# Kernel tuning notes

Hardware: AMD Instinct MI355X
Metric: run time of the kernel (lower is better)

## Reference

```python
import jax, jax.numpy as jnp
import numpy as np
from jax import lax

HEAD_DIM = 8          # attention_head_dim
EPS_ATTN = 1e-15
EPS_RMS = 1e-5
KPAD = 2              # kernel_size 5 -> padding 2


def setup_inputs() -> dict:
    key = jax.random.key(0)
    ks = jax.random.split(key, 9)
    B, C, H, W = 2, 1152, 64, 64
    inner = 1152                     # num_heads(144) * head_dim(8)
    ch3 = 3 * inner                  # 3456
    s = 0.02
    return {
        "hidden_states": jax.random.normal(ks[0], (B, C, H, W), jnp.float32),
        "Wq": jax.random.normal(ks[1], (inner, C), jnp.float32) * s,
        "Wk": jax.random.normal(ks[2], (inner, C), jnp.float32) * s,
        "Wv": jax.random.normal(ks[3], (inner, C), jnp.float32) * s,
        "proj_in_w": jax.random.normal(ks[4], (ch3, 1, 5, 5), jnp.float32) * s,   # depthwise 5x5
        "proj_out_w": jax.random.normal(ks[5], (ch3, HEAD_DIM, 1, 1), jnp.float32) * s,  # grouped 1x1, groups=3*heads
        "Wout": jax.random.normal(ks[6], (C, 2 * inner), jnp.float32) * s,
        "rms_w": jnp.ones((C,), jnp.float32),
        "rms_b": jnp.zeros((C,), jnp.float32),
    }


def reference(hidden_states, Wq, Wk, Wv, proj_in_w, proj_out_w, Wout, rms_w, rms_b):
    x = hidden_states
    B, C, H, W = x.shape
    xh = jnp.transpose(x, (0, 2, 3, 1))                      # BHWC
    q = xh @ Wq.T
    k = xh @ Wk.T
    v = xh @ Wv.T
    qkv = jnp.transpose(jnp.concatenate([q, k, v], axis=-1), (0, 3, 1, 2))  # B,3*inner,H,W
    ch = qkv.shape[1]
    # multiscale branch: depthwise 5x5 then grouped 1x1 (groups = 3*num_heads)
    ms = lax.conv_general_dilated(qkv, proj_in_w, (1, 1), [(KPAD, KPAD), (KPAD, KPAD)],
                                  dimension_numbers=("NCHW", "OIHW", "NCHW"),
                                  feature_group_count=ch)
    ms = lax.conv_general_dilated(ms, proj_out_w, (1, 1), [(0, 0), (0, 0)],
                                  dimension_numbers=("NCHW", "OIHW", "NCHW"),
                                  feature_group_count=ch // HEAD_DIM)
    hs = jnp.concatenate([qkv, ms], axis=1).astype(jnp.float32)   # B, 2*3*inner, H, W
    hs = hs.reshape(B, -1, 3 * HEAD_DIM, H * W)                   # B, G, 3d, N
    q2, k2, v2 = jnp.split(hs, 3, axis=2)                         # each B,G,d,N
    q2 = jax.nn.relu(q2)
    k2 = jax.nn.relu(k2)
    # linear attention: pad value with a ones row (for the normalizer)
    v_pad = jnp.concatenate([v2, jnp.ones_like(v2[:, :, :1])], axis=2)  # B,G,d+1,N
    scores = jnp.einsum("bgdn,bgen->bgde", v_pad, k2)             # B,G,d+1,d (tiny)
    out = jnp.einsum("bgde,bgen->bgdn", scores, q2)               # B,G,d+1,N
    out = out[:, :, :-1] / (out[:, :, -1:] + EPS_ATTN)            # normalize by last row
    out = out.reshape(B, -1, H, W)                                # B, 2*inner, H, W
    out = jnp.transpose(out, (0, 2, 3, 1)) @ Wout.T               # BHW,C_out
    # RMSNorm over channel (last) dim, with affine weight + bias
    ms2 = jnp.mean(out * out, axis=-1, keepdims=True)
    out = out * lax.rsqrt(ms2 + EPS_RMS) * rms_w + rms_b
    return jnp.transpose(out, (0, 3, 1, 2))
```

## Files before the change

### kernel.cpp

```cpp
#include <hip/hip_runtime.h>

typedef _Float16 f16;
typedef f16 f16x8 __attribute__((ext_vector_type(8)));
typedef float f32x16 __attribute__((ext_vector_type(16)));

#define NB 2
#define NC 1152
#define NHW 4096
#define NCH3 3456
#define NC2 2304

#define LO_SCALE 2048.0f
#define LO_INV (1.0f / 2048.0f)


__device__ __align__(16) f16 g_Wcat_h[(size_t)NCH3 * NC];
__device__ __align__(16) f16 g_Wcat_l[(size_t)NC * NC];
__device__ __align__(16) f16 g_WoutB_h[(size_t)NC * NC2];
__device__ __align__(16) f16 g_XT_h[(size_t)NB * NHW * NC];
__device__ __align__(16) f16 g_XT_l[(size_t)NB * NHW * NC];
__device__ __align__(16) f16 g_qkv[(size_t)NB * NCH3 * NHW];
__device__ __align__(16) f16 g_ms[(size_t)NB * NCH3 * NHW];
__device__ __align__(16) f16 g_attnT_h[(size_t)NB * NHW * NC2];
__device__ float g_part[NB * NHW];

__device__ __forceinline__ void gload16(const void* g, void* l) {
  __builtin_amdgcn_global_load_lds(
      (const __attribute__((address_space(1))) unsigned int*)g,
      (__attribute__((address_space(3))) unsigned int*)l, 16, 0, 0);
}

__device__ __forceinline__ void split_f16(float v, f16& h, f16& l) {
  h = (f16)v;
  l = (f16)((v - (float)h) * LO_SCALE);
}

__global__ __launch_bounds__(256) void convert_weights(
    const float* __restrict__ wq, const float* __restrict__ wk,
    const float* __restrict__ wv, const float* __restrict__ wout) {
  size_t idx = ((size_t)blockIdx.x * 256 + threadIdx.x) * 4;
  const size_t NWC = (size_t)NCH3 * NC;
  const size_t NWO = (size_t)NC * NC2;
  if (idx < NWC) {
    int p = (int)(idx / NC);
    int kk = (int)(idx % NC);
    int role = p / 1152, w = p % 1152;
    int g = w >> 3, r = w & 7;
    int c = g * 24 + role * 8 + r;
    const float* src = (c < 1152) ? wq + (size_t)c * NC + kk
                      : (c < 2304) ? wk + (size_t)(c - 1152) * NC + kk
                                   : wv + (size_t)(c - 2304) * NC + kk;
    if (p < 1152) {
#pragma unroll
      for (int j = 0; j < 4; ++j)
        split_f16(src[j], g_Wcat_h[idx + j], g_Wcat_l[idx + j]);
    } else {
#pragma unroll
      for (int j = 0; j < 4; ++j) g_Wcat_h[idx + j] = (f16)src[j];
    }
  } else {
    size_t k = idx - NWC;
    if (k < NWO) {
      const float* src = wout + k;
#pragma unroll
      for (int j = 0; j < 4; ++j) g_WoutB_h[k + j] = (f16)src[j];
    }
  }
}

__global__ __launch_bounds__(256) void transpose_x(const float* __restrict__ x) {
  __shared__ float tile[32][33];
  int z = blockIdx.z;
  int p0 = blockIdx.x * 32, c0 = blockIdx.y * 32;
  int tx = threadIdx.x, ty = threadIdx.y;
#pragma unroll
  for (int i = 0; i < 32; i += 8)
    tile[ty + i][tx] = x[((size_t)z * NC + c0 + ty + i) * NHW + p0 + tx];
  __syncthreads();
#pragma unroll
  for (int i = 0; i < 32; i += 8) {
    size_t o = ((size_t)z * NHW + p0 + ty + i) * NC + c0 + tx;
    split_f16(tile[tx][ty + i], g_XT_h[o], g_XT_l[o]);
  }
}


__device__ __forceinline__ void gemm1_split_body(char* smem, int bm, int bn, int bz) {
  const int tid = threadIdx.x;
  const int lane = tid & 63;
  const int wid = tid >> 6;
  const int wr = wid >> 2, wc = wid & 3;
  const size_t boff = (size_t)bz * ((size_t)NHW * NC);
  const f16* Bh = g_XT_h + boff;
  const f16* Bl = g_XT_l + boff;
  f16* Cb = g_qkv + (size_t)bz * ((size_t)NCH3 * NHW);
  const int srow = tid >> 2;
  const int skb = (((tid & 3) ^ ((srow >> 1) & 3)) * 8);
  const f16* gAh = g_Wcat_h + (size_t)(bm + srow) * NC + skb;
  const f16* gAl = g_Wcat_l + (size_t)(bm + srow) * NC + skb;
  const f16* gBh0 = Bh + (size_t)(bn + srow) * NC + skb;
  const f16* gBl0 = Bl + (size_t)(bn + srow) * NC + skb;
  const f16* gBh1 = Bh + (size_t)(bn + 128 + srow) * NC + skb;
  const f16* gBl1 = Bl + (size_t)(bn + 128 + srow) * NC + skb;
  const int ldso = tid * 16;

  f32x16 acc[2][2] = {};
  f32x16 acc2[2][2] = {};
  const int r31 = lane & 31;
  const int key = (r31 >> 1) & 3;
  const int kblk = lane >> 5;

#define BUF(b, off) (smem + (b) * 49152 + (off))
#define STAGE_S(buf, tile)                                      \
  do {                                                          \
    size_t ko = (size_t)(tile) * 32;                            \
    gload16(gAh + ko, BUF(buf, 0) + ldso);                      \
    gload16(gAl + ko, BUF(buf, 8192) + ldso);                   \
    gload16(gBh0 + ko, BUF(buf, 16384) + ldso);                 \
    gload16(gBh1 + ko, BUF(buf, 24576) + ldso);                 \
    gload16(gBl0 + ko, BUF(buf, 32768) + ldso);                 \
    gload16(gBl1 + ko, BUF(buf, 40960) + ldso);                 \
  } while (0)

#define COMPUTE_S(buf)                                                         \
  do {                                                                         \
    const f16* sAh = (const f16*)BUF(buf, 0);                                  \
    const f16* sAl = (const f16*)BUF(buf, 8192);                               \
    const f16* sBh = (const f16*)BUF(buf, 16384);                              \
    const f16* sBl = (const f16*)BUF(buf, 32768);                              \
    _Pragma("unroll") for (int kh = 0; kh < 2; ++kh) {                         \
      const int bsw = ((kh * 2 + kblk) ^ key) * 8;                             \
      f16x8 ah[2], al[2], bh[2], bl[2];                                        \
      _Pragma("unroll") for (int mb = 0; mb < 2; ++mb) {                       \
        int ro = (wr * 64 + mb * 32 + r31) * 32 + bsw;                         \
        ah[mb] = *(const f16x8*)(sAh + ro);                                    \
        al[mb] = *(const f16x8*)(sAl + ro);                                    \
      }                                                                        \
      _Pragma("unroll") for (int nb = 0; nb < 2; ++nb) {                       \
        int ro = (wc * 64 + nb * 32 + r31) * 32 + bsw;                         \
        bh[nb] = *(const f16x8*)(sBh + ro);                                    \
        bl[nb] = *(const f16x8*)(sBl + ro);                                    \
      }                                                                        \
      __builtin_amdgcn_s_setprio(1);                                           \
      _Pragma("unroll") for (int mb = 0; mb < 2; ++mb)                         \
        _Pragma("unroll") for (int nb = 0; nb < 2; ++nb) {                     \
          acc[mb][nb]  = __builtin_amdgcn_mfma_f32_32x32x16_f16(ah[mb], bh[nb], acc[mb][nb], 0, 0, 0);  \
          acc2[mb][nb] = __builtin_amdgcn_mfma_f32_32x32x16_f16(ah[mb], bl[nb], acc2[mb][nb], 0, 0, 0); \
          acc2[mb][nb] = __builtin_amdgcn_mfma_f32_32x32x16_f16(al[mb], bh[nb], acc2[mb][nb], 0, 0, 0); \
        }                                                                      \
      __builtin_amdgcn_s_setprio(0);                                           \
    }                                                                          \
  } while (0)

  const int NT = NC / 32;
  STAGE_S(0, 0);
  STAGE_S(1, 1);
  int cb = 0, sb = 2;
#pragma unroll 1
  for (int t = 0; t < NT - 1; ++t) {
    asm volatile("s_waitcnt vmcnt(6)" ::: "memory");
    __builtin_amdgcn_s_barrier();
    __builtin_amdgcn_sched_barrier(0);
    if (t + 2 < NT) STAGE_S(sb, t + 2);
    COMPUTE_S(cb);
    __builtin_amdgcn_sched_barrier(0);
    __builtin_amdgcn_s_barrier();
    cb = (cb == 2) ? 0 : cb + 1;
    sb = (sb == 2) ? 0 : sb + 1;
  }
  asm volatile("s_waitcnt vmcnt(0)" ::: "memory");
  __builtin_amdgcn_s_barrier();
  __builtin_amdgcn_sched_barrier(0);
  COMPUTE_S(cb);
#undef STAGE_S
#undef COMPUTE_S
#undef BUF
#pragma unroll
  for (int mb = 0; mb < 2; ++mb)
#pragma unroll
    for (int nb = 0; nb < 2; ++nb) {
      int col = bn + wc * 64 + nb * 32 + r31;
#pragma unroll
      for (int reg = 0; reg < 16; ++reg) {
        int row = bm + wr * 64 + mb * 32 + (reg & 3) + 8 * (reg >> 2) + 4 * (lane >> 5);
        Cb[(size_t)row * NHW + col] = (f16)(acc[mb][nb][reg] + acc2[mb][nb][reg] * LO_INV);
      }
    }
}

__device__ __forceinline__ void gemm1_plain_body(char* smem, int bm, int bn, int bz) {
  const int tid = threadIdx.x;
  const int lane = tid & 63;
  const int wid = tid >> 6;
  const int wr = wid >> 2, wc = wid & 3;
  const size_t boff = (size_t)bz * ((size_t)NHW * NC);
  const f16* Bh = g_XT_h + boff;
  f16* Cb = g_qkv + (size_t)bz * ((size_t)NCH3 * NHW);
  const int srow = tid >> 2;
  const int skb = (((tid & 3) ^ ((srow >> 1) & 3)) * 8);
  const f16* gA = g_Wcat_h + (size_t)(bm + srow) * NC + skb;
  const f16* gB0 = Bh + (size_t)(bn + srow) * NC + skb;
  const f16* gB1 = Bh + (size_t)(bn + 128 + srow) * NC + skb;
  const int ldso = tid * 16;

  f32x16 acc[2][2] = {};
  const int r31 = lane & 31;
  const int key = (r31 >> 1) & 3;
  const int kblk = lane >> 5;

#define BUF(b, off) (smem + (b) * 24576 + (off))
#define STAGE_Q(buf, tile)                                      \
  do {                                                          \
    size_t ko = (size_t)(tile) * 32;                            \
    gload16(gA + ko, BUF(buf, 0) + ldso);                       \
    gload16(gB0 + ko, BUF(buf, 8192) + ldso);                   \
    gload16(gB1 + ko, BUF(buf, 16384) + ldso);                  \
  } while (0)

#define COMPUTE_Q(buf)                                                         \
  do {                                                                         \
    const f16* sA = (const f16*)BUF(buf, 0);                                   \
    const f16* sB = (const f16*)BUF(buf, 8192);                                \
    _Pragma("unroll") for (int kh = 0; kh < 2; ++kh) {                         \
      const int bsw = ((kh * 2 + kblk) ^ key) * 8;                             \
      f16x8 af[2], bf[2];                                                      \
      _Pragma("unroll") for (int mb = 0; mb < 2; ++mb)                         \
        af[mb] = *(const f16x8*)(sA + (wr * 64 + mb * 32 + r31) * 32 + bsw);   \
      _Pragma("unroll") for (int nb = 0; nb < 2; ++nb)                         \
        bf[nb] = *(const f16x8*)(sB + (wc * 64 + nb * 32 + r31) * 32 + bsw);   \
      __builtin_amdgcn_s_setprio(1);                                           \
      _Pragma("unroll") for (int mb = 0; mb < 2; ++mb)                         \
        _Pragma("unroll") for (int nb = 0; nb < 2; ++nb)                       \
          acc[mb][nb] = __builtin_amdgcn_mfma_f32_32x32x16_f16(af[mb], bf[nb], acc[mb][nb], 0, 0, 0); \
      __builtin_amdgcn_s_setprio(0);                                           \
    }                                                                          \
  } while (0)

  const int NT = NC / 32;
  STAGE_Q(0, 0);
  STAGE_Q(1, 1);
  int cb = 0, sb = 2;
#pragma unroll 1
  for (int t = 0; t < NT - 1; ++t) {
    asm volatile("s_waitcnt vmcnt(3)" ::: "memory");
    __builtin_amdgcn_s_barrier();
    __builtin_amdgcn_sched_barrier(0);
    if (t + 2 < NT) STAGE_Q(sb, t + 2);
    COMPUTE_Q(cb);
    __builtin_amdgcn_sched_barrier(0);
    __builtin_amdgcn_s_barrier();
    cb = (cb == 2) ? 0 : cb + 1;
    sb = (sb == 2) ? 0 : sb + 1;
  }
  asm volatile("s_waitcnt vmcnt(0)" ::: "memory");
  __builtin_amdgcn_s_barrier();
  __builtin_amdgcn_sched_barrier(0);
  COMPUTE_Q(cb);
#undef STAGE_Q
#undef COMPUTE_Q
#undef BUF
#pragma unroll
  for (int mb = 0; mb < 2; ++mb)
#pragma unroll
    for (int nb = 0; nb < 2; ++nb) {
      int col = bn + wc * 64 + nb * 32 + r31;
#pragma unroll
      for (int reg = 0; reg < 16; ++reg) {
        int row = bm + wr * 64 + mb * 32 + (reg & 3) + 8 * (reg >> 2) + 4 * (lane >> 5);
        Cb[(size_t)row * NHW + col] = (f16)acc[mb][nb][reg];
      }
    }
}

__global__ __launch_bounds__(512, 1) void gemm1_kernel() {
  __shared__ __align__(16) char smem[147456];
  int bid = blockIdx.x;
  int swz = (bid & 7) * 108 + (bid >> 3);
  int bx = swz % 27, rem = swz / 27;
  int by = rem & 15, bz = rem >> 4;
  if (bx < 9)
    gemm1_split_body(smem, bx * 128, by * 256, bz);
  else
    gemm1_plain_body(smem, bx * 128, by * 256, bz);
}

template <int M, int N, int K>
__device__ __forceinline__ void gemm_body_plain(
    const f16* __restrict__ A, const f16* __restrict__ Bt,
    float* __restrict__ C, int bm, int bn, int bz) {
  __shared__ __align__(16) f16 sA[3][128 * 32];
  __shared__ __align__(16) f16 sB[3][128 * 32];
  const int tid = threadIdx.x;
  const int lane = tid & 63;
  const int wid = tid >> 6;
  const int wr = wid >> 1, wc = wid & 1;
  const f16* Bb = Bt + (size_t)bz * ((size_t)N * K);
  float* Cb = C + (size_t)bz * ((size_t)M * N);
  const int srow = tid >> 2;
  const int skb = (((tid & 3) ^ ((srow >> 1) & 3)) * 8);
  const f16* gA0 = A + (size_t)(bm + srow) * K + skb;
  const f16* gA1 = A + (size_t)(bm + 64 + srow) * K + skb;
  const f16* gB0 = Bb + (size_t)(bn + srow) * K + skb;
  const f16* gB1 = Bb + (size_t)(bn + 64 + srow) * K + skb;
  const int ldso = tid * 16;

  f32x16 acc[2][2] = {};
  const int r31 = lane & 31;
  const int key = (r31 >> 1) & 3;
  const int kblk = lane >> 5;

#define STAGE_P(buf, tile)                              \
  do {                                                  \
    size_t ko = (size_t)(tile) * 32;                    \
    gload16(gA0 + ko, (char*)sA[buf] + ldso);           \
    gload16(gA1 + ko, (char*)sA[buf] + 4096 + ldso);    \
    gload16(gB0 + ko, (char*)sB[buf] + ldso);           \
    gload16(gB1 + ko, (char*)sB[buf] + 4096 + ldso);    \
  } while (0)

#define COMPUTE_P(buf)                                                         \
  do {                                                                         \
    _Pragma("unroll") for (int kh = 0; kh < 2; ++kh) {                         \
      const int bsw = ((kh * 2 + kblk) ^ key) * 8;                             \
      f16x8 af[2], bf[2];                                                      \
      _Pragma("unroll") for (int mb = 0; mb < 2; ++mb)                         \
        af[mb] = *(const f16x8*)(sA[buf] + (wr * 64 + mb * 32 + r31) * 32 + bsw); \
      _Pragma("unroll") for (int nb = 0; nb < 2; ++nb)                         \
        bf[nb] = *(const f16x8*)(sB[buf] + (wc * 64 + nb * 32 + r31) * 32 + bsw); \
      __builtin_amdgcn_s_setprio(1);                                           \
      _Pragma("unroll") for (int mb = 0; mb < 2; ++mb)                         \
        _Pragma("unroll") for (int nb = 0; nb < 2; ++nb)                       \
          acc[mb][nb] = __builtin_amdgcn_mfma_f32_32x32x16_f16(af[mb], bf[nb], acc[mb][nb], 0, 0, 0); \
      __builtin_amdgcn_s_setprio(0);                                           \
    }                                                                          \
  } while (0)

  const int NT = K / 32;
  STAGE_P(0, 0);
  STAGE_P(1, 1);
  int cb = 0, sb = 2;
#pragma unroll 1
  for (int t = 0; t < NT - 1; ++t) {
    asm volatile("s_waitcnt vmcnt(4)" ::: "memory");
    __builtin_amdgcn_s_barrier();
    __builtin_amdgcn_sched_barrier(0);
    if (t + 2 < NT) STAGE_P(sb, t + 2);
    COMPUTE_P(cb);
    __builtin_amdgcn_sched_barrier(0);
    __builtin_amdgcn_s_barrier();
    cb = (cb == 2) ? 0 : cb + 1;
    sb = (sb == 2) ? 0 : sb + 1;
  }
  asm volatile("s_waitcnt vmcnt(0)" ::: "memory");
  __builtin_amdgcn_s_barrier();
  __builtin_amdgcn_sched_barrier(0);
  COMPUTE_P(cb);
#undef STAGE_P
#undef COMPUTE_P
#pragma unroll
  for (int nb = 0; nb < 2; ++nb) {
    int col = bn + wc * 64 + nb * 32 + r31;
    float csum = 0.f;
#pragma unroll
    for (int mb = 0; mb < 2; ++mb)
#pragma unroll
      for (int reg = 0; reg < 16; ++reg) {
        int row = bm + wr * 64 + mb * 32 + (reg & 3) + 8 * (reg >> 2) + 4 * (lane >> 5);
        float v = acc[mb][nb][reg];
        Cb[(size_t)row * N + col] = v;
        csum += v * v;
      }
    atomicAdd(&g_part[bz * NHW + col], csum);
  }
}

__global__ __launch_bounds__(256, 2) void gemm2_kernel(float* __restrict__ out) {
  int bid = blockIdx.x;
  int swz = (bid & 7) * (576 / 8) + (bid >> 3);
  int bx = swz % 9, rem = swz / 9;
  int by = rem & 31, bz = rem >> 5;
  gemm_body_plain<NC, NHW, NC2>(g_WoutB_h, g_attnT_h, out,
                                bx * 128, by * 128, bz);
}

__global__ __launch_bounds__(256) void conv_kernel(const float* __restrict__ wdw,
                                                   const float* __restrict__ wpw) {
  const int z = blockIdx.z, gg = blockIdx.y;
  const int pbase = (gg % 3) * 1152 + (gg / 3) * 8;
  const int px = blockIdx.x * 2048 + threadIdx.x * 8;
  const int h = px >> 6, w0 = px & 63;
  const f16* base = g_qkv + ((size_t)z * NCH3 + pbase) * NHW;

  float dw[8][8];
#pragma unroll
  for (int ci = 0; ci < 8; ++ci) {
    const float* wd = wdw + (gg * 8 + ci) * 25;
    const f16* srcc = base + (size_t)ci * NHW;
    float acc[8] = {};
#pragma unroll
    for (int dy = -2; dy <= 2; ++dy) {
      int hh = h + dy;
      if (hh < 0 || hh > 63) continue;
      const f16* row = srcc + hh * 64;
      f16x8 Lv = {}, Rv = {};
      if (w0 >= 8) Lv = *(const f16x8*)(row + w0 - 8);
      f16x8 Mv = *(const f16x8*)(row + w0);
      if (w0 <= 48) Rv = *(const f16x8*)(row + w0 + 8);
      float c[24];
#pragma unroll
      for (int i = 0; i < 8; ++i) {
        c[i] = (float)Lv[i];
        c[8 + i] = (float)Mv[i];
        c[16 + i] = (float)Rv[i];
      }
      const float* wrow = wd + (dy + 2) * 5;
#pragma unroll
      for (int dx = 0; dx < 5; ++dx) {
        float wv = wrow[dx];
#pragma unroll
        for (int j = 0; j < 8; ++j) acc[j] += c[6 + j + dx] * wv;
      }
    }
#pragma unroll
    for (int j = 0; j < 8; ++j) dw[ci][j] = acc[j];
  }
#pragma unroll
  for (int o = 0; o < 8; ++o) {
    const float* wp = wpw + (size_t)(gg * 8 + o) * 8;
    float out[8] = {};
#pragma unroll
    for (int i = 0; i < 8; ++i) {
      float wv = wp[i];
#pragma unroll
      for (int j = 0; j < 8; ++j) out[j] += wv * dw[i][j];
    }
    f16x8 ov;
#pragma unroll
    for (int j = 0; j < 8; ++j) ov[j] = (f16)out[j];
    *(f16x8*)(g_ms + ((size_t)z * NCH3 + pbase + o) * NHW + px) = ov;
  }
}

__global__ __launch_bounds__(256) void attn_kernel() {
  int g = blockIdx.x;
  int z = blockIdx.y;
  int tid = threadIdx.x;
  const f16* buf = (g < 144) ? g_qkv : g_ms;
  int gq = (g < 144) ? g : g - 144;
  const f16* qp = buf + ((size_t)z * NCH3 + gq * 8) * NHW;
  const f16* kp = buf + ((size_t)z * NCH3 + 1152 + gq * 8) * NHW;
  const f16* vp = buf + ((size_t)z * NCH3 + 2304 + gq * 8) * NHW;

  float s[9][8];
#pragma unroll
  for (int d = 0; d < 9; ++d)
#pragma unroll
    for (int e = 0; e < 8; ++e) s[d][e] = 0.f;

  for (int p0 = tid * 8; p0 < NHW; p0 += 2048) {
    f16x8 kx[8], vx[8];
#pragma unroll
    for (int e = 0; e < 8; ++e) kx[e] = *(const f16x8*)(kp + (size_t)e * NHW + p0);
#pragma unroll
    for (int d = 0; d < 8; ++d) vx[d] = *(const f16x8*)(vp + (size_t)d * NHW + p0);
#pragma unroll
    for (int j = 0; j < 8; ++j) {
      float kv[8], vv[8];
#pragma unroll
      for (int e = 0; e < 8; ++e) kv[e] = fmaxf((float)kx[e][j], 0.f);
#pragma unroll
      for (int d = 0; d < 8; ++d) vv[d] = (float)vx[d][j];
#pragma unroll
      for (int e = 0; e < 8; ++e) {
#pragma unroll
        for (int d = 0; d < 8; ++d) s[d][e] += vv[d] * kv[e];
        s[8][e] += kv[e];
      }
    }
  }
#pragma unroll
  for (int d = 0; d < 9; ++d)
#pragma unroll
    for (int e = 0; e < 8; ++e) {
      float v = s[d][e];
#pragma unroll
      for (int off = 32; off > 0; off >>= 1) v += __shfl_xor(v, off, 64);
      s[d][e] = v;
    }
  __shared__ float sred[4][72];
  __shared__ float sc[72];
  int w = tid >> 6, lane = tid & 63;
  if (lane == 0) {
#pragma unroll
    for (int d = 0; d < 9; ++d)
#pragma unroll
      for (int e = 0; e < 8; ++e) sred[w][d * 8 + e] = s[d][e];
  }
  __syncthreads();
  if (tid < 72) sc[tid] = sred[0][tid] + sred[1][tid] + sred[2][tid] + sred[3][tid];
  __syncthreads();
  float scl[9][8];
#pragma unroll
  for (int d = 0; d < 9; ++d)
#pragma unroll
    for (int e = 0; e < 8; ++e) scl[d][e] = sc[d * 8 + e];

  for (int p0 = tid * 8; p0 < NHW; p0 += 2048) {
    f16x8 qx[8];
#pragma unroll
    for (int e = 0; e < 8; ++e) qx[e] = *(const f16x8*)(qp + (size_t)e * NHW + p0);
#pragma unroll
    for (int j = 0; j < 8; ++j) {
      float qv[8];
#pragma unroll
      for (int e = 0; e < 8; ++e) qv[e] = fmaxf((float)qx[e][j], 0.f);
      float o[9];
#pragma unroll
      for (int d = 0; d < 9; ++d) {
        float a = 0.f;
#pragma unroll
        for (int e = 0; e < 8; ++e) a += scl[d][e] * qv[e];
        o[d] = a;
      }
      float r = 1.f / (o[8] + 1e-15f);
      f16x8 oh;
#pragma unroll
      for (int d = 0; d < 8; ++d) oh[d] = (f16)(o[d] * r);
      *(f16x8*)(g_attnT_h + ((size_t)z * NHW + p0 + j) * NC2 + g * 8) = oh;
    }
  }
}

__global__ __launch_bounds__(256) void rms_zero() {
  g_part[blockIdx.x * 256 + threadIdx.x] = 0.f;
}
__global__ __launch_bounds__(256) void rms_norm(float* __restrict__ y,
                                                const float* __restrict__ w,
                                                const float* __restrict__ b) {
  size_t i = ((size_t)blockIdx.x * 256 + threadIdx.x) * 4;
  float4 v = *(const float4*)(y + i);
  int p = (int)(i & (NHW - 1));
  int c = (int)((i >> 12) % NC);
  int z = (int)(i / ((size_t)NC * NHW));
  const float inv = 1.0f / NC;
  float wc = w[c], bc = b[c];
  const float* pp = &g_part[z * NHW + p];
  v.x = v.x * rsqrtf(pp[0] * inv + 1e-5f) * wc + bc;
  v.y = v.y * rsqrtf(pp[1] * inv + 1e-5f) * wc + bc;
  v.z = v.z * rsqrtf(pp[2] * inv + 1e-5f) * wc + bc;
  v.w = v.w * rsqrtf(pp[3] * inv + 1e-5f) * wc + bc;
  *(float4*)(y + i) = v;
}

extern "C" void kernel_launch(void* const* d_in, const int* in_sizes, int n_in,
                              void* d_out, int out_size, void* d_ws, size_t ws_size,
                              hipStream_t stream) {
  const float* x = (const float*)d_in[0];
  const float* wq = (const float*)d_in[1];
  const float* wk = (const float*)d_in[2];
  const float* wv = (const float*)d_in[3];
  const float* wdw = (const float*)d_in[4];
  const float* wpw = (const float*)d_in[5];
  const float* wout = (const float*)d_in[6];
  const float* rw = (const float*)d_in[7];
  const float* rb = (const float*)d_in[8];
  float* y = (float*)d_out;

  convert_weights<<<6480, 256, 0, stream>>>(wq, wk, wv, wout);
  transpose_x<<<dim3(128, 36, 2), dim3(32, 8), 0, stream>>>(x);
  gemm1_kernel<<<864, 512, 0, stream>>>();
  conv_kernel<<<dim3(2, 432, 2), 256, 0, stream>>>(wdw, wpw);
  attn_kernel<<<dim3(288, 2), 256, 0, stream>>>();
  rms_zero<<<32, 256, 0, stream>>>();
  gemm2_kernel<<<576, 256, 0, stream>>>(y);
  rms_norm<<<9216, 256, 0, stream>>>(y, rw, rb);
}
```

Baseline: 399.0 us.

## Split gemm1 into separate split-precision and plain kernels with larger plain tiles

Replaces the single fused gemm1 kernel, which branched per block between the split-precision (hi/lo) body and the plain f16 body, with two separate launches. The plain kernel now uses 256x256 tiles instead of 128x256, so each block does twice the MFMA work per B load and the grid shrinks. Its K loop is reorganised into two half-phases, with the A and B stage loads interleaved between the MFMA groups. Splitting removes load imbalance and branch divergence between block types, but serialises the two kernels and leaves 288-block grids that may underfill the device.

```diff
diff --git a/kernel.cpp b/kernel.cpp
--- a/kernel.cpp
+++ b/kernel.cpp
@@ -84,8 +84,13 @@
   }
 }
 
-
-__device__ __forceinline__ void gemm1_split_body(char* smem, int bm, int bn, int bz) {
+__global__ __launch_bounds__(512, 1) void gemm1s_kernel() {
+  __shared__ __align__(16) char smem[147456];
+  int bid = blockIdx.x;
+  int swz = (bid & 7) * 36 + (bid >> 3);
+  int bx = swz % 9, rem = swz / 9;
+  int bm = bx * 128, bn = (rem & 15) * 256, bz = rem >> 4;
+
   const int tid = threadIdx.x;
   const int lane = tid & 63;
   const int wid = tid >> 6;
@@ -188,100 +193,104 @@
     }
 }
 
-__device__ __forceinline__ void gemm1_plain_body(char* smem, int bm, int bn, int bz) {
+__global__ __launch_bounds__(512, 1) void gemm1p_kernel() {
+  __shared__ __align__(16) f16 sA[3][256 * 32];
+  __shared__ __align__(16) f16 sB[3][256 * 32];
+  int bid = blockIdx.x;
+  int swz = (bid & 7) * 36 + (bid >> 3);
+  int bx = swz % 9, rem = swz / 9;
+  int bmG = 1152 + bx * 256;
+  int bn = (rem & 15) * 256;
+  int bz = rem >> 4;
+
   const int tid = threadIdx.x;
   const int lane = tid & 63;
   const int wid = tid >> 6;
   const int wr = wid >> 2, wc = wid & 3;
-  const size_t boff = (size_t)bz * ((size_t)NHW * NC);
-  const f16* Bh = g_XT_h + boff;
+  const f16* Bb = g_XT_h + (size_t)bz * ((size_t)NHW * NC);
   f16* Cb = g_qkv + (size_t)bz * ((size_t)NCH3 * NHW);
   const int srow = tid >> 2;
   const int skb = (((tid & 3) ^ ((srow >> 1) & 3)) * 8);
-  const f16* gA = g_Wcat_h + (size_t)(bm + srow) * NC + skb;
-  const f16* gB0 = Bh + (size_t)(bn + srow) * NC + skb;
-  const f16* gB1 = Bh + (size_t)(bn + 128 + srow) * NC + skb;
+  const f16* gA0 = g_Wcat_h + (size_t)(bmG + srow) * NC + skb;
+  const f16* gA1 = g_Wcat_h + (size_t)(bmG + 128 + srow) * NC + skb;
+  const f16* gB0 = Bb + (size_t)(bn + srow) * NC + skb;
+  const f16* gB1 = Bb + (size_t)(bn + 128 + srow) * NC + skb;
   const int ldso = tid * 16;
 
-  f32x16 acc[2][2] = {};
+  f32x16 acc[4][2] = {};
   const int r31 = lane & 31;
   const int key = (r31 >> 1) & 3;
   const int kblk = lane >> 5;
 
-#define BUF(b, off) (smem + (b) * 24576 + (off))
-#define STAGE_Q(buf, tile)                                      \
+#define STG_A(buf, tile)                                        \
   do {                                                          \
     size_t ko = (size_t)(tile) * 32;                            \
-    gload16(gA + ko, BUF(buf, 0) + ldso);                       \
-    gload16(gB0 + ko, BUF(buf, 8192) + ldso);                   \
-    gload16(gB1 + ko, BUF(buf, 16384) + ldso);                  \
-  } while (0)
-
-#define COMPUTE_Q(buf)                                                         \
+    gload16(gA0 + ko, (char*)sA[buf] + ldso);                   \
+    gload16(gA1 + ko, (char*)sA[buf] + 8192 + ldso);            \
+  } while (0)
+#define STG_B(buf, tile)                                        \
+  do {                                                          \
+    size_t ko = (size_t)(tile) * 32;                            \
+    gload16(gB0 + ko, (char*)sB[buf] + ldso);                   \
+    gload16(gB1 + ko, (char*)sB[buf] + 8192 + ldso);            \
+  } while (0)
+
+#define FPHASE(buf, ks, STG)                                                   \
   do {                                                                         \
-    const f16* sA = (const f16*)BUF(buf, 0);                                   \
-    const f16* sB = (const f16*)BUF(buf, 8192);                                \
-    _Pragma("unroll") for (int kh = 0; kh < 2; ++kh) {                         \
-      const int bsw = ((kh * 2 + kblk) ^ key) * 8;                             \
-      f16x8 af[2], bf[2];                                                      \
-      _Pragma("unroll") for (int mb = 0; mb < 2; ++mb)                         \
-        af[mb] = *(const f16x8*)(sA + (wr * 64 + mb * 32 + r31) * 32 + bsw);   \
+    STG;                                                                       \
+    const int bsw = ((ks) * 2 + kblk) * 8;                                     \
+    f16x8 af[4], bf[2];                                                        \
+    _Pragma("unroll") for (int ma = 0; ma < 4; ++ma) {                         \
+      int row = wr * 128 + ma * 32 + r31;                                      \
+      af[ma] = *(const f16x8*)(sA[buf] + row * 32 + ((bsw >> 3) ^ key) * 8);   \
+    }                                                                          \
+    _Pragma("unroll") for (int nb = 0; nb < 2; ++nb) {                         \
+      int row = wc * 64 + nb * 32 + r31;                                       \
+      bf[nb] = *(const f16x8*)(sB[buf] + row * 32 + ((bsw >> 3) ^ key) * 8);   \
+    }                                                                          \
+    __builtin_amdgcn_s_setprio(1);                                             \
+    _Pragma("unroll") for (int ma = 0; ma < 4; ++ma)                           \
       _Pragma("unroll") for (int nb = 0; nb < 2; ++nb)                         \
-        bf[nb] = *(const f16x8*)(sB + (wc * 64 + nb * 32 + r31) * 32 + bsw);   \
-      __builtin_amdgcn_s_setprio(1);                                           \
-      _Pragma("unroll") for (int mb = 0; mb < 2; ++mb)                         \
-        _Pragma("unroll") for (int nb = 0; nb < 2; ++nb)                       \
-          acc[mb][nb] = __builtin_amdgcn_mfma_f32_32x32x16_f16(af[mb], bf[nb], acc[mb][nb], 0, 0, 0); \
-      __builtin_amdgcn_s_setprio(0);                                           \
-    }                                                                          \
+        acc[ma][nb] = __builtin_amdgcn_mfma_f32_32x32x16_f16(af[ma], bf[nb], acc[ma][nb], 0, 0, 0); \
+    __builtin_amdgcn_s_setprio(0);                                             \
   } while (0)
 
   const int NT = NC / 32;
-  STAGE_Q(0, 0);
-  STAGE_Q(1, 1);
-  int cb = 0, sb = 2;
+  STG_A(0, 0); STG_B(0, 0);
+  STG_A(1, 1); STG_B(1, 1);
+  int cb = 0;
 #pragma unroll 1
-  for (int t = 0; t < NT - 1; ++t) {
-    asm volatile("s_waitcnt vmcnt(3)" ::: "memory");
+  for (int t = 0; t < NT - 2; ++t) {
+    asm volatile("s_waitcnt vmcnt(4)" ::: "memory");
     __builtin_amdgcn_s_barrier();
-    __builtin_amdgcn_sched_barrier(0);
-    if (t + 2 < NT) STAGE_Q(sb, t + 2);
-    COMPUTE_Q(cb);
-    __builtin_amdgcn_sched_barrier(0);
-    __builtin_amdgcn_s_barrier();
+    int pb = cb + 2; if (pb >= 3) pb -= 3;
+    FPHASE(cb, 0, STG_A(pb, t + 2));
+    FPHASE(cb, 1, STG_B(pb, t + 2));
     cb = (cb == 2) ? 0 : cb + 1;
-    sb = (sb == 2) ? 0 : sb + 1;
-  }
+  }
+  asm volatile("s_waitcnt vmcnt(4)" ::: "memory");
+  __builtin_amdgcn_s_barrier();
+  FPHASE(cb, 0, (void)0);
+  FPHASE(cb, 1, (void)0);
+  cb = (cb == 2) ? 0 : cb + 1;
   asm volatile("s_waitcnt vmcnt(0)" ::: "memory");
   __builtin_amdgcn_s_barrier();
-  __builtin_amdgcn_sched_barrier(0);
-  COMPUTE_Q(cb);
-#undef STAGE_Q
-#undef COMPUTE_Q
-#undef BUF
-#pragma unroll
-  for (int mb = 0; mb < 2; ++mb)
+  FPHASE(cb, 0, (void)0);
+  FPHASE(cb, 1, (void)0);
+#undef STG_A
+#undef STG_B
+#undef FPHASE
+#pragma unroll
+  for (int ma = 0; ma < 4; ++ma)
 #pragma unroll
     for (int nb = 0; nb < 2; ++nb) {
       int col = bn + wc * 64 + nb * 32 + r31;
 #pragma unroll
       for (int reg = 0; reg < 16; ++reg) {
-        int row = bm + wr * 64 + mb * 32 + (reg & 3) + 8 * (reg >> 2) + 4 * (lane >> 5);
-        Cb[(size_t)row * NHW + col] = (f16)acc[mb][nb][reg];
-      }
-    }
-}
-
-__global__ __launch_bounds__(512, 1) void gemm1_kernel() {
-  __shared__ __align__(16) char smem[147456];
-  int bid = blockIdx.x;
-  int swz = (bid & 7) * 108 + (bid >> 3);
-  int bx = swz % 27, rem = swz / 27;
-  int by = rem & 15, bz = rem >> 4;
-  if (bx < 9)
-    gemm1_split_body(smem, bx * 128, by * 256, bz);
-  else
-    gemm1_plain_body(smem, bx * 128, by * 256, bz);
+        int row = bmG + wr * 128 + ma * 32 + (reg & 3) + 8 * (reg >> 2) + 4 * (lane >> 5);
+        Cb[(size_t)row * NHW + col] = (f16)acc[ma][nb][reg];
+      }
+    }
 }
 
 template <int M, int N, int K>
@@ -568,7 +577,8 @@
 
   convert_weights<<<6480, 256, 0, stream>>>(wq, wk, wv, wout);
   transpose_x<<<dim3(128, 36, 2), dim3(32, 8), 0, stream>>>(x);
-  gemm1_kernel<<<864, 512, 0, stream>>>();
+  gemm1s_kernel<<<288, 512, 0, stream>>>();
+  gemm1p_kernel<<<288, 512, 0, stream>>>();
   conv_kernel<<<dim3(2, 432, 2), 256, 0, stream>>>(wdw, wpw);
   attn_kernel<<<dim3(288, 2), 256, 0, stream>>>();
   rms_zero<<<32, 256, 0, stream>>>();
```

Result: slower. 476.1 us (+19.3%).
